# Optimization experiments

Hardware: AMD Instinct MI355X
Metric: run time of the kernel (lower is better)

## Reference

```python
import jax, jax.numpy as jnp
import numpy as np

S = 7                # feature map size
A = 12               # anchors per cell
N = S * S * A        # 588 total anchors
ANCHOR_SCALES = [0.3, 0.5, 0.7, 0.9]
ANCHOR_RATIOS = [0.7, 1.0, 1.3]
CONF_THR = 0.3
NMS_THR = 0.5
MAX_DET = 100
BN_EPS = 1e-5
DN = ('NCHW', 'OIHW', 'NCHW')


def _anchors():
    g = (jnp.arange(S, dtype=jnp.float32) + 0.5) / S
    cx, cy = jnp.meshgrid(g, g, indexing='ij')
    centers = jnp.stack([cx, cy], -1).reshape(-1, 2)                 # [49,2]
    sc = jnp.asarray(ANCHOR_SCALES, jnp.float32)[:, None]
    rt = jnp.sqrt(jnp.asarray(ANCHOR_RATIOS, jnp.float32))[None, :]
    ws = (sc * rt).reshape(-1)
    hs = (sc / rt).reshape(-1)
    deltas = jnp.stack([-ws, -hs, ws, hs], -1) * 0.5                 # [12,4]
    return (jnp.concatenate([centers, centers], -1)[:, None, :] + deltas[None]).reshape(-1, 4)


def _conv(x, w, b, pad):
    y = jax.lax.conv_general_dilated(x, w, (1, 1), [(pad, pad), (pad, pad)], dimension_numbers=DN)
    return y + b[None, :, None, None]


def _bn_relu(x, g, be, mu, var):
    inv = g * jax.lax.rsqrt(var + BN_EPS)
    return jax.nn.relu(x * inv[None, :, None, None] + (be - mu * inv)[None, :, None, None])


def _decode(box_pred, anchors):
    ac = (anchors[:, :2] + anchors[:, 2:]) * 0.5
    asz = anchors[:, 2:] - anchors[:, :2]
    pc = box_pred[..., :2] * asz + ac
    ps = jnp.exp(box_pred[..., 2:]) * asz
    return jnp.concatenate([pc - ps * 0.5, pc + ps * 0.5], -1)


def _iou(b):
    area = (b[:, 2] - b[:, 0]) * (b[:, 3] - b[:, 1])
    lt = jnp.maximum(b[:, None, :2], b[None, :, :2])
    rb = jnp.minimum(b[:, None, 2:], b[None, :, 2:])
    wh = jnp.clip(rb - lt, 0.0)
    inter = wh[..., 0] * wh[..., 1]
    return inter / (area[:, None] + area[None, :] - inter + 1e-9)


def _nms_single(boxes, scores):
    # greedy NMS, fixed-shape: sort by score, sequentially suppress, pad to MAX_DET
    order = jnp.argsort(-scores)
    bs = boxes[order]
    ss = scores[order]
    vs = ss > CONF_THR
    iou = _iou(bs)
    idx = jnp.arange(N)

    def body(suppr, i):
        keep = vs[i] & jnp.logical_not(suppr[i])
        suppr = suppr | (keep & (iou[i] > NMS_THR) & (idx > i))
        return suppr, keep

    _, keep = jax.lax.scan(body, jnp.zeros((N,), bool), idx)
    kept = jnp.where(keep, ss, -1.0)           # scores in (0,1), -1 is a safe sentinel
    top_s, top_i = jax.lax.top_k(kept, MAX_DET)
    valid = top_s > 0.0
    out_b = jnp.where(valid[:, None], bs[top_i], 0.0)
    out_s = jnp.where(valid, top_s, 0.0)
    return jnp.concatenate([out_b, out_s[:, None], valid.astype(jnp.float32)[:, None]], -1)


def _forward(features, w1, b1, g1, be1, mu1, var1, w2, b2, g2, be2, mu2, var2,
             w3, b3, g3, be3, mu3, var3, w4, b4, g4, be4, mu4, var4,
             w_cls, b_cls, w_box, b_box):
    x = _bn_relu(_conv(features, w1, b1, 0), g1, be1, mu1, var1)   # fpn 1x1
    x = _bn_relu(_conv(x, w2, b2, 1), g2, be2, mu2, var2)          # fpn 3x3
    x = _bn_relu(_conv(x, w3, b3, 1), g3, be3, mu3, var3)          # det_conv 1
    x = _bn_relu(_conv(x, w4, b4, 1), g4, be4, mu4, var4)          # det_conv 2
    B = features.shape[0]
    box = _conv(x, w_box, b_box, 1).transpose(0, 2, 3, 1).reshape(B, -1, 4)
    conf = jax.nn.sigmoid(_conv(x, w_cls, b_cls, 1)).transpose(0, 2, 3, 1).reshape(B, -1)
    boxes = _decode(box, _anchors())
    return jax.vmap(_nms_single)(boxes, conf)   # [B, MAX_DET, 6] = box(4)+score+valid


def setup_inputs() -> dict:
    key = jax.random.key(0)
    ks = iter(jax.random.split(key, 64))
    B = 256
    d = {'features': jax.random.normal(next(ks), (B, 512, S, S), jnp.float32)}
    for n, o, i, k in [('1', 256, 512, 1), ('2', 256, 256, 3), ('3', 256, 256, 3), ('4', 256, 256, 3)]:
        d['w' + n] = 0.01 * jax.random.normal(next(ks), (o, i, k, k), jnp.float32)
        d['b' + n] = jnp.zeros((o,), jnp.float32)
        d['g' + n] = 1.0 + 0.1 * jax.random.normal(next(ks), (o,), jnp.float32)
        d['be' + n] = 0.05 * jax.random.normal(next(ks), (o,), jnp.float32)
        d['mu' + n] = 0.1 * jax.random.normal(next(ks), (o,), jnp.float32)
        d['var' + n] = jax.random.uniform(next(ks), (o,), jnp.float32, 0.5, 1.5)
    d['w_cls'] = 0.01 * jax.random.normal(next(ks), (A, 256, 3, 3), jnp.float32)
    d['b_cls'] = jnp.zeros((A,), jnp.float32)
    d['w_box'] = 0.01 * jax.random.normal(next(ks), (4 * A, 256, 3, 3), jnp.float32)
    d['b_box'] = jnp.zeros((4 * A,), jnp.float32)
    return d


def reference(features, w1, b1, g1, be1, mu1, var1, w2, b2, g2, be2, mu2, var2,
              w3, b3, g3, be3, mu3, var3, w4, b4, g4, be4, mu4, var4,
              w_cls, b_cls, w_box, b_box):
    return _forward(features, w1, b1, g1, be1, mu1, var1, w2, b2, g2, be2, mu2, var2,
                    w3, b3, g3, be3, mu3, var3, w4, b4, g4, be4, mu4, var4,
                    w_cls, b_cls, w_box, b_box)
```

## Files before the change

### kernel.cpp

```cpp
#include <hip/hip_runtime.h>
#include <cmath>
#include <cstdint>

#define NPOS 49
#define NANCH 588

__global__ void transpose_all(
    const float* __restrict__ w1, const float* __restrict__ w2,
    const float* __restrict__ w3, const float* __restrict__ w4,
    const float* __restrict__ wb, const float* __restrict__ wc,
    float* __restrict__ w1t, float* __restrict__ w2t, float* __restrict__ w3t,
    float* __restrict__ w4t, float* __restrict__ wbt, float* __restrict__ wct) {
  int idx = blockIdx.x * blockDim.x + threadIdx.x;
  if (idx < 131072) {
    int o = idx / 512, c = idx % 512;
    w1t[((c >> 2) * 256 + o) * 4 + (c & 3)] = w1[idx];
    return;
  }
  idx -= 131072;
  if (idx < 589824) {
    int o = idx / 2304, ck = idx % 2304, c = ck / 9, k = ck - c * 9;
    w2t[(c * 256 + o) * 12 + k] = w2[idx]; return;
  }
  idx -= 589824;
  if (idx < 589824) {
    int o = idx / 2304, ck = idx % 2304, c = ck / 9, k = ck - c * 9;
    w3t[(c * 256 + o) * 12 + k] = w3[idx]; return;
  }
  idx -= 589824;
  if (idx < 589824) {
    int o = idx / 2304, ck = idx % 2304, c = ck / 9, k = ck - c * 9;
    w4t[(c * 256 + o) * 12 + k] = w4[idx]; return;
  }
  idx -= 589824;
  if (idx < 110592) { int o = idx / 2304, ck = idx % 2304; wbt[ck * 48 + o] = wb[idx]; return; }
  idx -= 110592;
  if (idx < 27648)  { int o = idx / 2304, ck = idx % 2304; wct[ck * 12 + o] = wc[idx]; return; }
}

__global__ __launch_bounds__(512, 1) void conv1x1_bn(
    const float* __restrict__ in, const float* __restrict__ wt_f,
    const float* __restrict__ bias, const float* __restrict__ gg,
    const float* __restrict__ be, const float* __restrict__ mu,
    const float* __restrict__ var, float* __restrict__ out) {
  __shared__ float smem[512 * 52];
  const int b = blockIdx.x, t = threadIdx.x;
  const int slot = t & 127, cg = t >> 7;
  const int o0 = slot, o1 = slot + 128;
  const float* inb = in + (size_t)b * (512 * NPOS);
  const float4* wq = (const float4*)wt_f;
  const int q0 = cg * 32;
  float4 wca = wq[q0 * 256 + o0];
  float4 wcb = wq[q0 * 256 + o1];
  for (int i = t; i < 512 * NPOS; i += 512) {
    int c = i / NPOS, p = i - c * NPOS;
    smem[c * 52 + p] = inb[i];
  }
  float acc0[NPOS], acc1[NPOS];
#pragma unroll
  for (int p = 0; p < NPOS; ++p) { acc0[p] = 0.f; acc1[p] = 0.f; }
  __syncthreads();
  for (int q = q0; q < q0 + 32; ++q) {
    int nq = (q + 1 < q0 + 32) ? q + 1 : q;
    float4 wna = wq[nq * 256 + o0];
    float4 wnb = wq[nq * 256 + o1];
#pragma unroll
    for (int j = 0; j < 4; ++j) {
      float wa = (j == 0) ? wca.x : (j == 1) ? wca.y : (j == 2) ? wca.z : wca.w;
      float wb2 = (j == 0) ? wcb.x : (j == 1) ? wcb.y : (j == 2) ? wcb.z : wcb.w;
      const float* row = smem + (q * 4 + j) * 52;
      const float4* tr = (const float4*)row;
#pragma unroll
      for (int jj = 0; jj < 12; ++jj) {
        float4 qv = tr[jj];
        acc0[4 * jj + 0] = fmaf(wa, qv.x, acc0[4 * jj + 0]);
        acc0[4 * jj + 1] = fmaf(wa, qv.y, acc0[4 * jj + 1]);
        acc0[4 * jj + 2] = fmaf(wa, qv.z, acc0[4 * jj + 2]);
        acc0[4 * jj + 3] = fmaf(wa, qv.w, acc0[4 * jj + 3]);
        acc1[4 * jj + 0] = fmaf(wb2, qv.x, acc1[4 * jj + 0]);
        acc1[4 * jj + 1] = fmaf(wb2, qv.y, acc1[4 * jj + 1]);
        acc1[4 * jj + 2] = fmaf(wb2, qv.z, acc1[4 * jj + 2]);
        acc1[4 * jj + 3] = fmaf(wb2, qv.w, acc1[4 * jj + 3]);
      }
      float s48 = row[48];
      acc0[48] = fmaf(wa, s48, acc0[48]);
      acc1[48] = fmaf(wb2, s48, acc1[48]);
    }
    wca = wna; wcb = wnb;
  }
  __syncthreads();
  float* P0 = smem;
  float* P1 = smem + 12544;
  if (cg == 1) {
#pragma unroll
    for (int p = 0; p < NPOS; ++p) { P0[(slot * 2 + 0) * NPOS + p] = acc0[p]; P0[(slot * 2 + 1) * NPOS + p] = acc1[p]; }
  }
  if (cg == 3) {
#pragma unroll
    for (int p = 0; p < NPOS; ++p) { P1[(slot * 2 + 0) * NPOS + p] = acc0[p]; P1[(slot * 2 + 1) * NPOS + p] = acc1[p]; }
  }
  __syncthreads();
  if (cg == 0) {
#pragma unroll
    for (int p = 0; p < NPOS; ++p) { acc0[p] += P0[(slot * 2 + 0) * NPOS + p]; acc1[p] += P0[(slot * 2 + 1) * NPOS + p]; }
  }
  if (cg == 2) {
#pragma unroll
    for (int p = 0; p < NPOS; ++p) { acc0[p] += P1[(slot * 2 + 0) * NPOS + p]; acc1[p] += P1[(slot * 2 + 1) * NPOS + p]; }
  }
  __syncthreads();
  if (cg == 2) {
#pragma unroll
    for (int p = 0; p < NPOS; ++p) { P0[(slot * 2 + 0) * NPOS + p] = acc0[p]; P0[(slot * 2 + 1) * NPOS + p] = acc1[p]; }
  }
  __syncthreads();
  if (cg == 0) {
    float sc0 = gg[o0] / sqrtf(var[o0] + 1e-5f);
    float ad0 = (bias[o0] - mu[o0]) * sc0 + be[o0];
    float sc1 = gg[o1] / sqrtf(var[o1] + 1e-5f);
    float ad1 = (bias[o1] - mu[o1]) * sc1 + be[o1];
#pragma unroll
    for (int p = 0; p < NPOS; ++p) {
      float v0 = (acc0[p] + P0[(slot * 2 + 0) * NPOS + p]) * sc0 + ad0;
      float v1 = (acc1[p] + P0[(slot * 2 + 1) * NPOS + p]) * sc1 + ad1;
      P1[o0 * NPOS + p] = v0 > 0.f ? v0 : 0.f;
      P1[o1 * NPOS + p] = v1 > 0.f ? v1 : 0.f;
    }
  }
  __syncthreads();
  float* outb = out + (size_t)b * (256 * NPOS);
  for (int i = t; i < 256 * NPOS; i += 512) outb[i] = P1[i];
}

#define LOADROW2(dst, base, yy)                                         \
  do {                                                                  \
    const float4* q4_ = (const float4*)((base) + (yy) * 8);             \
    float4 a_ = q4_[0], b_ = q4_[1];                                    \
    dst[0] = 0.f;                                                       \
    dst[1] = a_.x; dst[2] = a_.y; dst[3] = a_.z; dst[4] = a_.w;         \
    dst[5] = b_.x; dst[6] = b_.y; dst[7] = b_.z; dst[8] = b_.w;         \
  } while (0)

#define FMA9(accbase, rt, rc, rb)                                       \
  do {                                                                  \
    _Pragma("unroll")                                                   \
    for (int x = 0; x < 7; ++x) {                                       \
      float s = acc[(accbase) + x];                                     \
      s = fmaf(wa0.x, rt[x],     s);                                    \
      s = fmaf(wa0.y, rt[x + 1], s);                                    \
      s = fmaf(wa0.z, rt[x + 2], s);                                    \
      s = fmaf(wa0.w, rc[x],     s);                                    \
      s = fmaf(wa1.x, rc[x + 1], s);                                    \
      s = fmaf(wa1.y, rc[x + 2], s);                                    \
      s = fmaf(wa1.z, rb[x],     s);                                    \
      s = fmaf(wa1.w, rb[x + 1], s);                                    \
      s = fmaf(wa2.x, rb[x + 2], s);                                    \
      acc[(accbase) + x] = s;                                           \
    }                                                                   \
  } while (0)

__global__ __launch_bounds__(512, 2) void conv3x3_bn(
    const float* __restrict__ in, const float* __restrict__ wt,
    const float* __restrict__ bias, const float* __restrict__ gg,
    const float* __restrict__ be, const float* __restrict__ mu,
    const float* __restrict__ var, float* __restrict__ out) {
  __shared__ float smem[256 * 56];
  const int blk = blockIdx.x, t = threadIdx.x;
  const int b = blk >> 1, oh = blk & 1;
  const int slot = t & 127, cg = t >> 7;
  const int og = oh * 128 + slot;
  const float* inb = in + (size_t)b * (256 * NPOS);
  float4* z4 = (float4*)smem;
  for (int i = t; i < 3584; i += 512) z4[i] = make_float4(0.f, 0.f, 0.f, 0.f);
  const int c0 = cg * 64;
  const float4* wv4 = (const float4*)wt;
  float4 wa0 = wv4[(c0 * 256 + og) * 3 + 0];
  float4 wa1 = wv4[(c0 * 256 + og) * 3 + 1];
  float4 wa2 = wv4[(c0 * 256 + og) * 3 + 2];
  __syncthreads();
  for (int i = t; i < 256 * NPOS; i += 512) {
    int c = i / NPOS, p = i - c * NPOS, y = p / 7, x = p - y * 7;
    smem[c * 56 + y * 8 + x] = inb[i];
  }
  float acc[NPOS];
#pragma unroll
  for (int p = 0; p < NPOS; ++p) acc[p] = 0.f;
  __syncthreads();
  for (int cl = 0; cl < 64; ++cl) {
    const int c = c0 + cl;
    const int cn = (cl + 1 < 64) ? c + 1 : c;
    float4 na0 = wv4[(cn * 256 + og) * 3 + 0];
    float4 na1 = wv4[(cn * 256 + og) * 3 + 1];
    float4 na2 = wv4[(cn * 256 + og) * 3 + 2];
    const float* tb = smem + c * 56;
    float R0[9], R1[9], R2[9];
    LOADROW2(R0, tb, 0);
    LOADROW2(R1, tb, 1);
#pragma unroll
    for (int x = 0; x < 7; ++x) {
      float s = acc[x];
      s = fmaf(wa0.w, R0[x],     s);
      s = fmaf(wa1.x, R0[x + 1], s);
      s = fmaf(wa1.y, R0[x + 2], s);
      s = fmaf(wa1.z, R1[x],     s);
      s = fmaf(wa1.w, R1[x + 1], s);
      s = fmaf(wa2.x, R1[x + 2], s);
      acc[x] = s;
    }
    LOADROW2(R2, tb, 2);
    FMA9(7, R0, R1, R2);
    LOADROW2(R0, tb, 3);
    FMA9(14, R1, R2, R0);
    LOADROW2(R1, tb, 4);
    FMA9(21, R2, R0, R1);
    LOADROW2(R2, tb, 5);
    FMA9(28, R0, R1, R2);
    LOADROW2(R0, tb, 6);
    FMA9(35, R1, R2, R0);
#pragma unroll
    for (int x = 0; x < 7; ++x) {
      float s = acc[42 + x];
      s = fmaf(wa0.x, R2[x],     s);
      s = fmaf(wa0.y, R2[x + 1], s);
      s = fmaf(wa0.z, R2[x + 2], s);
      s = fmaf(wa0.w, R0[x],     s);
      s = fmaf(wa1.x, R0[x + 1], s);
      s = fmaf(wa1.y, R0[x + 2], s);
      acc[42 + x] = s;
    }
    wa0 = na0; wa1 = na1; wa2 = na2;
  }
  __syncthreads();
  float* P0 = smem;
  float* P1 = smem + 6272;
  if (cg == 1) { for (int p = 0; p < NPOS; ++p) P0[slot * NPOS + p] = acc[p]; }
  if (cg == 3) { for (int p = 0; p < NPOS; ++p) P1[slot * NPOS + p] = acc[p]; }
  __syncthreads();
  if (cg == 0) { for (int p = 0; p < NPOS; ++p) acc[p] += P0[slot * NPOS + p]; }
  if (cg == 2) { for (int p = 0; p < NPOS; ++p) acc[p] += P1[slot * NPOS + p]; }
  __syncthreads();
  if (cg == 2) { for (int p = 0; p < NPOS; ++p) P0[slot * NPOS + p] = acc[p]; }
  __syncthreads();
  if (cg == 0) {
    float scale = gg[og] / sqrtf(var[og] + 1e-5f);
    float add = (bias[og] - mu[og]) * scale + be[og];
#pragma unroll
    for (int p = 0; p < NPOS; ++p) {
      float v = (acc[p] + P0[slot * NPOS + p]) * scale + add;
      P1[slot * NPOS + p] = v > 0.f ? v : 0.f;
    }
  }
  __syncthreads();
  float* outb = out + (size_t)b * (256 * NPOS) + oh * (128 * NPOS);
  for (int i = t; i < 128 * NPOS; i += 512) outb[i] = P1[i];
}

#define LOADROW(dst, base, rr)                                          \
  do {                                                                  \
    const float4* q4_ = (const float4*)((base) + (rr) * 12);            \
    float4 q0_ = q4_[0], q1_ = q4_[1], q2_ = q4_[2];                    \
    dst[0] = q0_.x; dst[1] = q0_.y; dst[2] = q0_.z; dst[3] = q0_.w;     \
    dst[4] = q1_.x; dst[5] = q1_.y; dst[6] = q1_.z; dst[7] = q1_.w;     \
    dst[8] = q2_.x;                                                     \
  } while (0)

__global__ __launch_bounds__(512, 2) void heads_decode(
    const float* __restrict__ in, const float* __restrict__ wbt,
    const float* __restrict__ wct, const float* __restrict__ bb,
    const float* __restrict__ bc, float* __restrict__ BXg,
    float* __restrict__ SCg) {
  __shared__ float smem[256 * 108];
  const int b = blockIdx.x, t = threadIdx.x;
  for (int i = t; i < 256 * 108; i += 512) smem[i] = 0.f;
  __syncthreads();
  const float* inb = in + (size_t)b * (256 * NPOS);
  for (int i = t; i < 256 * NPOS; i += 512) {
    int c = i / NPOS, p = i - c * NPOS, y = p / 7, x = p - y * 7;
    smem[c * 108 + (y + 1) * 12 + (x + 1)] = inb[i];
  }
  __syncthreads();
  float acc[NPOS];
#pragma unroll
  for (int p = 0; p < NPOS; ++p) acc[p] = 0.f;
  int o = 0, cg = 0;
  if (t < 480) {
    o = t % 60; cg = t / 60;
    const float* wbase; int wstr;
    if (o < 48) { wbase = wbt + o; wstr = 48; }
    else        { wbase = wct + (o - 48); wstr = 12; }
    const int c0 = cg * 32;
    float wc_[9];
#pragma unroll
    for (int k = 0; k < 9; ++k) wc_[k] = wbase[(c0 * 9 + k) * wstr];
    for (int c = c0; c < c0 + 32; ++c) {
      int cn = (c + 1 < c0 + 32) ? c + 1 : c;
      float wn_[9];
#pragma unroll
      for (int k = 0; k < 9; ++k) wn_[k] = wbase[(cn * 9 + k) * wstr];
      const float* tb = smem + c * 108;
      float R[3][9];
      LOADROW(R[0], tb, 0);
      LOADROW(R[1], tb, 1);
#pragma unroll
      for (int y = 0; y < 7; ++y) {
        LOADROW(R[(y + 2) % 3], tb, y + 2);
        const float* r0 = R[y % 3];
        const float* r1 = R[(y + 1) % 3];
        const float* r2 = R[(y + 2) % 3];
#pragma unroll
        for (int x = 0; x < 7; ++x) {
          float s = acc[y * 7 + x];
          s = fmaf(wc_[0], r0[x], s);
          s = fmaf(wc_[1], r0[x + 1], s);
          s = fmaf(wc_[2], r0[x + 2], s);
          s = fmaf(wc_[3], r1[x], s);
          s = fmaf(wc_[4], r1[x + 1], s);
          s = fmaf(wc_[5], r1[x + 2], s);
          s = fmaf(wc_[6], r2[x], s);
          s = fmaf(wc_[7], r2[x + 1], s);
          s = fmaf(wc_[8], r2[x + 2], s);
          acc[y * 7 + x] = s;
        }
      }
#pragma unroll
      for (int k = 0; k < 9; ++k) wc_[k] = wn_[k];
    }
  }
  __syncthreads();
  float* part = smem;
  float* H = smem + 7 * 2940;
  if (t < 480 && cg > 0) {
#pragma unroll
    for (int p = 0; p < NPOS; ++p) part[(cg - 1) * 2940 + o * NPOS + p] = acc[p];
  }
  __syncthreads();
  if (t < 60) {
    float bsum = (o < 48) ? bb[o] : bc[o - 48];
#pragma unroll
    for (int p = 0; p < NPOS; ++p) {
      float v = acc[p] + bsum;
      for (int g = 0; g < 7; ++g) v += part[g * 2940 + o * NPOS + p];
      H[o * NPOS + p] = v;
    }
  }
  __syncthreads();
  const float scl[4] = {0.3f, 0.5f, 0.7f, 0.9f};
  const float rat[3] = {0.7f, 1.0f, 1.3f};
  for (int n = t; n < NANCH; n += 512) {
    int p = n / 12, a = n - p * 12;
    int ph = p / 7, pw = p - ph * 7;
    float cx = (ph + 0.5f) / 7.0f;
    float cy = (pw + 0.5f) / 7.0f;
    int s = a / 3, r = a - s * 3;
    float rt = sqrtf(rat[r]);
    float wsz = scl[s] * rt, hsz = scl[s] / rt;
    float x1 = cx + (-wsz) * 0.5f, y1 = cy + (-hsz) * 0.5f;
    float x2 = cx + wsz * 0.5f,    y2 = cy + hsz * 0.5f;
    float acx = (x1 + x2) * 0.5f,  acy = (y1 + y2) * 0.5f;
    float asx = x2 - x1,           asy = y2 - y1;
    float bp0 = H[(a * 4 + 0) * NPOS + p];
    float bp1 = H[(a * 4 + 1) * NPOS + p];
    float bp2 = H[(a * 4 + 2) * NPOS + p];
    float bp3 = H[(a * 4 + 3) * NPOS + p];
    float pcx = bp0 * asx + acx;
    float pcy = bp1 * asy + acy;
    float psx = expf(bp2) * asx;
    float psy = expf(bp3) * asy;
    float* bx = BXg + (size_t)b * (NANCH * 4) + n * 4;
    bx[0] = pcx - psx * 0.5f;
    bx[1] = pcy - psy * 0.5f;
    bx[2] = pcx + psx * 0.5f;
    bx[3] = pcy + psy * 0.5f;
    float lg = H[(48 + a) * NPOS + p];
    SCg[(size_t)b * NANCH + n] = 1.0f / (1.0f + expf(-lg));
  }
}

__device__ inline unsigned long long shfl64(unsigned long long v, int lane) {
  int lo = __shfl((int)(unsigned)(v & 0xffffffffULL), lane, 64);
  int hi = __shfl((int)(unsigned)(v >> 32), lane, 64);
  return ((unsigned long long)(unsigned)hi << 32) | (unsigned)lo;
}

__global__ __launch_bounds__(512, 4) void nms_kernel(
    const float* __restrict__ BXg, const float* __restrict__ SCg,
    float* __restrict__ out) {
  __shared__ float smem[16576];
  unsigned long long* KEY = (unsigned long long*)smem;
  float* SB  = smem + 1176;
  float* SSc = smem + 3528;
  float* AR  = smem + 4116;
  unsigned long long* ADJ = (unsigned long long*)(smem + 4704);
  int* KEEP = (int*)(smem + 16464);
  int* CNT  = (int*)(smem + 16564);
  const int b = blockIdx.x, t = threadIdx.x;
  const float* scb = SCg + (size_t)b * NANCH;
  const float4* bxb = (const float4*)(BXg + (size_t)b * (NANCH * 4));
  for (int i = t; i < NANCH; i += 512) {
    unsigned u = __float_as_uint(scb[i]);
    u = (u & 0x80000000u) ? ~u : (u | 0x80000000u);
    u = ~u;
    KEY[i] = ((unsigned long long)u << 32) | (unsigned)i;
  }
  __syncthreads();
  for (int i = t; i < NANCH; i += 512) {
    unsigned long long k = KEY[i];
    int rank = 0;
    for (int j = 0; j < NANCH; ++j) rank += (KEY[j] < k) ? 1 : 0;
    float4 bx = bxb[i];
    ((float4*)SB)[rank] = bx;
    SSc[rank] = scb[i];
    AR[rank] = (bx.z - bx.x) * (bx.w - bx.y);
  }
  __syncthreads();
  const float4* SB4 = (const float4*)SB;
  for (int task = t; task < NANCH * 10; task += 512) {
    int i = task % NANCH, w = task / NANCH;
    float4 a = SB4[i];
    float aar = AR[i];
    int jbase = w * 64;
    int jend = NANCH - jbase; if (jend > 64) jend = 64;
    unsigned long long bits = 0;
    for (int bi = 0; bi < jend; ++bi) {
      int j = jbase + bi;
      float4 bb = SB4[j];
      float ltx = fmaxf(a.x, bb.x), lty = fmaxf(a.y, bb.y);
      float rbx = fminf(a.z, bb.z), rby = fminf(a.w, bb.w);
      float wx = rbx - ltx; wx = wx > 0.f ? wx : 0.f;
      float wy = rby - lty; wy = wy > 0.f ? wy : 0.f;
      float inter = wx * wy;
      float iou = inter / (aar + AR[j] - inter + 1e-9f);
      if (iou > 0.5f) bits |= (1ULL << bi);
    }
    ADJ[i * 10 + w] = bits;
  }
  __syncthreads();
  if (t < 64) {
    unsigned long long valid = 0, supp = 0;
    if (t < 10) {
      int jbase = t * 64;
      int jend = NANCH - jbase; if (jend > 64) jend = 64;
      for (int k = 0; k < jend; ++k)
        valid |= (unsigned long long)(SSc[jbase + k] > 0.3f ? 1 : 0) << k;
    }
    int cnt = 0;
    for (int w = 0; w < 10 && cnt < 100; ++w) {
      unsigned long long cur = shfl64(valid, w) & ~shfl64(supp, w);
      while (cur && cnt < 100) {
        int bpos = (int)__builtin_ctzll(cur);
        int i = w * 64 + bpos;
        if (t == 0) KEEP[cnt] = i;
        cnt++;
        unsigned long long a = (t < 10) ? ADJ[i * 10 + t] : 0ULL;
        if (t < w) a = 0ULL;
        else if (t == w) a &= ~((2ULL << bpos) - 1ULL);
        supp |= a;
        unsigned long long aw = shfl64(a, w);
        cur &= ~aw;
        cur &= ~(1ULL << bpos);
      }
    }
    if (t == 0) *CNT = cnt;
  }
  __syncthreads();
  int cnt = *CNT;
  if (t < 100) {
    float4 bx = make_float4(0.f, 0.f, 0.f, 0.f);
    float s = 0.f, vld = 0.f;
    if (t < cnt) {
      int i = KEEP[t];
      bx = SB4[i];
      s = SSc[i];
      vld = 1.f;
    }
    float* ob = out + (size_t)b * 600 + t * 6;
    ob[0] = bx.x; ob[1] = bx.y; ob[2] = bx.z; ob[3] = bx.w;
    ob[4] = s;    ob[5] = vld;
  }
}

extern "C" void kernel_launch(void* const* d_in, const int* in_sizes, int n_in,
                              void* d_out, int out_size, void* d_ws, size_t ws_size,
                              hipStream_t stream) {
  const float* feat = (const float*)d_in[0];
  const float* w1  = (const float*)d_in[1];
  const float* b1  = (const float*)d_in[2];
  const float* g1  = (const float*)d_in[3];
  const float* be1 = (const float*)d_in[4];
  const float* mu1 = (const float*)d_in[5];
  const float* v1  = (const float*)d_in[6];
  const float* w2  = (const float*)d_in[7];
  const float* b2  = (const float*)d_in[8];
  const float* g2  = (const float*)d_in[9];
  const float* be2 = (const float*)d_in[10];
  const float* mu2 = (const float*)d_in[11];
  const float* v2  = (const float*)d_in[12];
  const float* w3  = (const float*)d_in[13];
  const float* b3  = (const float*)d_in[14];
  const float* g3  = (const float*)d_in[15];
  const float* be3 = (const float*)d_in[16];
  const float* mu3 = (const float*)d_in[17];
  const float* v3  = (const float*)d_in[18];
  const float* w4  = (const float*)d_in[19];
  const float* b4  = (const float*)d_in[20];
  const float* g4  = (const float*)d_in[21];
  const float* be4 = (const float*)d_in[22];
  const float* mu4 = (const float*)d_in[23];
  const float* v4  = (const float*)d_in[24];
  const float* wcls = (const float*)d_in[25];
  const float* bcls = (const float*)d_in[26];
  const float* wbox = (const float*)d_in[27];
  const float* bbox = (const float*)d_in[28];

  const int B = in_sizes[0] / (512 * NPOS);
  float* ws  = (float*)d_ws;
  size_t xsz = (size_t)B * 256 * NPOS;
  float* xa  = ws;
  float* xb  = xa + xsz;
  float* w1t = xb + xsz;
  float* w2t = w1t + 131072;
  float* w3t = w2t + 786432;
  float* w4t = w3t + 786432;
  float* wbt = w4t + 786432;
  float* wct = wbt + 110592;
  float* BXg = wct + 27648;
  float* SCg = BXg + (size_t)B * (NANCH * 4);

  transpose_all<<<(2038784 + 255) / 256, 256, 0, stream>>>(
      w1, w2, w3, w4, wbox, wcls, w1t, w2t, w3t, w4t, wbt, wct);
  conv1x1_bn<<<B, 512, 0, stream>>>(feat, w1t, b1, g1, be1, mu1, v1, xa);
  conv3x3_bn<<<2 * B, 512, 0, stream>>>(xa, w2t, b2, g2, be2, mu2, v2, xb);
  conv3x3_bn<<<2 * B, 512, 0, stream>>>(xb, w3t, b3, g3, be3, mu3, v3, xa);
  conv3x3_bn<<<2 * B, 512, 0, stream>>>(xa, w4t, b4, g4, be4, mu4, v4, xb);
  heads_decode<<<B, 512, 0, stream>>>(xb, wbt, wct, bbox, bcls, BXg, SCg);
  nms_kernel<<<B, 512, 0, stream>>>(BXg, SCg, (float*)d_out);
}
```

Measured before the change: 848.6 us.

## Split conv1x1 and heads kernels across two blocks per image, pin occupancy

The 1x1 conv is now split by output-channel half and the heads/decode kernel by spatial row half, so both launch two blocks per image instead of one. This roughly halves registers and shared memory per block. All conv kernels also get a fixed waves-per-EU occupancy attribute. The extra parallelism should fill more CUs when the batch is small. The cost is that the 1x1 conv and the heads kernel each read their input twice, and the heads reduction now needs more synchronised steps.

Result: no change. 851.5 us (+0.3%).

```diff
diff --git a/kernel.cpp b/kernel.cpp
--- a/kernel.cpp
+++ b/kernel.cpp
@@ -38,98 +38,76 @@
   if (idx < 27648)  { int o = idx / 2304, ck = idx % 2304; wct[ck * 12 + o] = wc[idx]; return; }
 }
 
-__global__ __launch_bounds__(512, 1) void conv1x1_bn(
+__global__ __launch_bounds__(512) __attribute__((amdgpu_waves_per_eu(4, 4)))
+void conv1x1_bn(
     const float* __restrict__ in, const float* __restrict__ wt_f,
     const float* __restrict__ bias, const float* __restrict__ gg,
     const float* __restrict__ be, const float* __restrict__ mu,
     const float* __restrict__ var, float* __restrict__ out) {
-  __shared__ float smem[512 * 52];
-  const int b = blockIdx.x, t = threadIdx.x;
+  __shared__ float smem[256 * 52];
+  const int blk = blockIdx.x, t = threadIdx.x;
+  const int b = blk >> 1, oh = blk & 1;
   const int slot = t & 127, cg = t >> 7;
-  const int o0 = slot, o1 = slot + 128;
+  const int og = oh * 128 + slot;
   const float* inb = in + (size_t)b * (512 * NPOS);
   const float4* wq = (const float4*)wt_f;
-  const int q0 = cg * 32;
-  float4 wca = wq[q0 * 256 + o0];
-  float4 wcb = wq[q0 * 256 + o1];
-  for (int i = t; i < 512 * NPOS; i += 512) {
-    int c = i / NPOS, p = i - c * NPOS;
-    smem[c * 52 + p] = inb[i];
-  }
-  float acc0[NPOS], acc1[NPOS];
-#pragma unroll
-  for (int p = 0; p < NPOS; ++p) { acc0[p] = 0.f; acc1[p] = 0.f; }
-  __syncthreads();
-  for (int q = q0; q < q0 + 32; ++q) {
-    int nq = (q + 1 < q0 + 32) ? q + 1 : q;
-    float4 wna = wq[nq * 256 + o0];
-    float4 wnb = wq[nq * 256 + o1];
-#pragma unroll
-    for (int j = 0; j < 4; ++j) {
-      float wa = (j == 0) ? wca.x : (j == 1) ? wca.y : (j == 2) ? wca.z : wca.w;
-      float wb2 = (j == 0) ? wcb.x : (j == 1) ? wcb.y : (j == 2) ? wcb.z : wcb.w;
-      const float* row = smem + (q * 4 + j) * 52;
-      const float4* tr = (const float4*)row;
-#pragma unroll
-      for (int jj = 0; jj < 12; ++jj) {
-        float4 qv = tr[jj];
-        acc0[4 * jj + 0] = fmaf(wa, qv.x, acc0[4 * jj + 0]);
-        acc0[4 * jj + 1] = fmaf(wa, qv.y, acc0[4 * jj + 1]);
-        acc0[4 * jj + 2] = fmaf(wa, qv.z, acc0[4 * jj + 2]);
-        acc0[4 * jj + 3] = fmaf(wa, qv.w, acc0[4 * jj + 3]);
-        acc1[4 * jj + 0] = fmaf(wb2, qv.x, acc1[4 * jj + 0]);
-        acc1[4 * jj + 1] = fmaf(wb2, qv.y, acc1[4 * jj + 1]);
-        acc1[4 * jj + 2] = fmaf(wb2, qv.z, acc1[4 * jj + 2]);
-        acc1[4 * jj + 3] = fmaf(wb2, qv.w, acc1[4 * jj + 3]);
+  float acc[NPOS];
+#pragma unroll
+  for (int p = 0; p < NPOS; ++p) acc[p] = 0.f;
+  for (int h = 0; h < 2; ++h) {
+    __syncthreads();
+    for (int i = t; i < 256 * NPOS; i += 512) {
+      int c = i / NPOS, p = i - c * NPOS;
+      smem[c * 52 + p] = inb[(h * 256 + c) * NPOS + p];
+    }
+    __syncthreads();
+    const int q0 = h * 64 + cg * 16;
+    float4 wcur = wq[q0 * 256 + og];
+    for (int q = q0; q < q0 + 16; ++q) {
+      int nq = (q + 1 < q0 + 16) ? q + 1 : q;
+      float4 wnxt = wq[nq * 256 + og];
+      const int clb = (q - h * 64) * 4;
+#pragma unroll
+      for (int j = 0; j < 4; ++j) {
+        float wv = (j == 0) ? wcur.x : (j == 1) ? wcur.y : (j == 2) ? wcur.z : wcur.w;
+        const float* row = smem + (clb + j) * 52;
+        const float4* tr = (const float4*)row;
+#pragma unroll
+        for (int jj = 0; jj < 12; ++jj) {
+          float4 qv = tr[jj];
+          acc[4 * jj + 0] = fmaf(wv, qv.x, acc[4 * jj + 0]);
+          acc[4 * jj + 1] = fmaf(wv, qv.y, acc[4 * jj + 1]);
+          acc[4 * jj + 2] = fmaf(wv, qv.z, acc[4 * jj + 2]);
+          acc[4 * jj + 3] = fmaf(wv, qv.w, acc[4 * jj + 3]);
+        }
+        acc[48] = fmaf(wv, row[48], acc[48]);
       }
-      float s48 = row[48];
-      acc0[48] = fmaf(wa, s48, acc0[48]);
-      acc1[48] = fmaf(wb2, s48, acc1[48]);
-    }
-    wca = wna; wcb = wnb;
+      wcur = wnxt;
+    }
   }
   __syncthreads();
   float* P0 = smem;
-  float* P1 = smem + 12544;
-  if (cg == 1) {
-#pragma unroll
-    for (int p = 0; p < NPOS; ++p) { P0[(slot * 2 + 0) * NPOS + p] = acc0[p]; P0[(slot * 2 + 1) * NPOS + p] = acc1[p]; }
-  }
-  if (cg == 3) {
-#pragma unroll
-    for (int p = 0; p < NPOS; ++p) { P1[(slot * 2 + 0) * NPOS + p] = acc0[p]; P1[(slot * 2 + 1) * NPOS + p] = acc1[p]; }
-  }
+  float* P1 = smem + 6272;
+  if (cg == 1) { for (int p = 0; p < NPOS; ++p) P0[slot * NPOS + p] = acc[p]; }
+  if (cg == 3) { for (int p = 0; p < NPOS; ++p) P1[slot * NPOS + p] = acc[p]; }
+  __syncthreads();
+  if (cg == 0) { for (int p = 0; p < NPOS; ++p) acc[p] += P0[slot * NPOS + p]; }
+  if (cg == 2) { for (int p = 0; p < NPOS; ++p) acc[p] += P1[slot * NPOS + p]; }
+  __syncthreads();
+  if (cg == 2) { for (int p = 0; p < NPOS; ++p) P0[slot * NPOS + p] = acc[p]; }
   __syncthreads();
   if (cg == 0) {
-#pragma unroll
-    for (int p = 0; p < NPOS; ++p) { acc0[p] += P0[(slot * 2 + 0) * NPOS + p]; acc1[p] += P0[(slot * 2 + 1) * NPOS + p]; }
-  }
-  if (cg == 2) {
-#pragma unroll
-    for (int p = 0; p < NPOS; ++p) { acc0[p] += P1[(slot * 2 + 0) * NPOS + p]; acc1[p] += P1[(slot * 2 + 1) * NPOS + p]; }
-  }
-  __syncthreads();
-  if (cg == 2) {
-#pragma unroll
-    for (int p = 0; p < NPOS; ++p) { P0[(slot * 2 + 0) * NPOS + p] = acc0[p]; P0[(slot * 2 + 1) * NPOS + p] = acc1[p]; }
-  }
-  __syncthreads();
-  if (cg == 0) {
-    float sc0 = gg[o0] / sqrtf(var[o0] + 1e-5f);
-    float ad0 = (bias[o0] - mu[o0]) * sc0 + be[o0];
-    float sc1 = gg[o1] / sqrtf(var[o1] + 1e-5f);
-    float ad1 = (bias[o1] - mu[o1]) * sc1 + be[o1];
+    float scale = gg[og] / sqrtf(var[og] + 1e-5f);
+    float add = (bias[og] - mu[og]) * scale + be[og];
 #pragma unroll
     for (int p = 0; p < NPOS; ++p) {
-      float v0 = (acc0[p] + P0[(slot * 2 + 0) * NPOS + p]) * sc0 + ad0;
-      float v1 = (acc1[p] + P0[(slot * 2 + 1) * NPOS + p]) * sc1 + ad1;
-      P1[o0 * NPOS + p] = v0 > 0.f ? v0 : 0.f;
-      P1[o1 * NPOS + p] = v1 > 0.f ? v1 : 0.f;
-    }
-  }
-  __syncthreads();
-  float* outb = out + (size_t)b * (256 * NPOS);
-  for (int i = t; i < 256 * NPOS; i += 512) outb[i] = P1[i];
+      float v = (acc[p] + P0[slot * NPOS + p]) * scale + add;
+      P1[slot * NPOS + p] = v > 0.f ? v : 0.f;
+    }
+  }
+  __syncthreads();
+  float* outb = out + (size_t)b * (256 * NPOS) + oh * (128 * NPOS);
+  for (int i = t; i < 128 * NPOS; i += 512) outb[i] = P1[i];
 }
 
 #define LOADROW2(dst, base, yy)                                         \
@@ -159,7 +137,8 @@
     }                                                                   \
   } while (0)
 
-__global__ __launch_bounds__(512, 2) void conv3x3_bn(
+__global__ __launch_bounds__(512) __attribute__((amdgpu_waves_per_eu(4, 4)))
+void conv3x3_bn(
     const float* __restrict__ in, const float* __restrict__ wt,
     const float* __restrict__ bias, const float* __restrict__ gg,
     const float* __restrict__ be, const float* __restrict__ mu,
@@ -255,33 +234,45 @@
   for (int i = t; i < 128 * NPOS; i += 512) outb[i] = P1[i];
 }
 
-#define LOADROW(dst, base, rr)                                          \
+#define HFMA9(accbase, rt, rc, rb)                                      \
   do {                                                                  \
-    const float4* q4_ = (const float4*)((base) + (rr) * 12);            \
-    float4 q0_ = q4_[0], q1_ = q4_[1], q2_ = q4_[2];                    \
-    dst[0] = q0_.x; dst[1] = q0_.y; dst[2] = q0_.z; dst[3] = q0_.w;     \
-    dst[4] = q1_.x; dst[5] = q1_.y; dst[6] = q1_.z; dst[7] = q1_.w;     \
-    dst[8] = q2_.x;                                                     \
+    _Pragma("unroll")                                                   \
+    for (int x = 0; x < 7; ++x) {                                       \
+      float s = acc[(accbase) + x];                                     \
+      s = fmaf(wc_[0], rt[x],     s);                                   \
+      s = fmaf(wc_[1], rt[x + 1], s);                                   \
+      s = fmaf(wc_[2], rt[x + 2], s);                                   \
+      s = fmaf(wc_[3], rc[x],     s);                                   \
+      s = fmaf(wc_[4], rc[x + 1], s);                                   \
+      s = fmaf(wc_[5], rc[x + 2], s);                                   \
+      s = fmaf(wc_[6], rb[x],     s);                                   \
+      s = fmaf(wc_[7], rb[x + 1], s);                                   \
+      s = fmaf(wc_[8], rb[x + 2], s);                                   \
+      acc[(accbase) + x] = s;                                           \
+    }                                                                   \
   } while (0)
 
-__global__ __launch_bounds__(512, 2) void heads_decode(
+__global__ __launch_bounds__(512) __attribute__((amdgpu_waves_per_eu(4, 4)))
+void heads_decode(
     const float* __restrict__ in, const float* __restrict__ wbt,
     const float* __restrict__ wct, const float* __restrict__ bb,
     const float* __restrict__ bc, float* __restrict__ BXg,
     float* __restrict__ SCg) {
-  __shared__ float smem[256 * 108];
-  const int b = blockIdx.x, t = threadIdx.x;
-  for (int i = t; i < 256 * 108; i += 512) smem[i] = 0.f;
+  __shared__ float smem[14720];
+  const int blk = blockIdx.x, t = threadIdx.x;
+  const int b = blk >> 1, pg = blk & 1;
+  float4* z4 = (float4*)smem;
+  for (int i = t; i < 3584; i += 512) z4[i] = make_float4(0.f, 0.f, 0.f, 0.f);
   __syncthreads();
   const float* inb = in + (size_t)b * (256 * NPOS);
   for (int i = t; i < 256 * NPOS; i += 512) {
     int c = i / NPOS, p = i - c * NPOS, y = p / 7, x = p - y * 7;
-    smem[c * 108 + (y + 1) * 12 + (x + 1)] = inb[i];
-  }
-  __syncthreads();
-  float acc[NPOS];
-#pragma unroll
-  for (int p = 0; p < NPOS; ++p) acc[p] = 0.f;
+    smem[c * 56 + y * 8 + x] = inb[i];
+  }
+  __syncthreads();
+  float acc[28];
+#pragma unroll
+  for (int p = 0; p < 28; ++p) acc[p] = 0.f;
   int o = 0, cg = 0;
   if (t < 480) {
     o = t % 60; cg = t / 60;
@@ -297,29 +288,45 @@
       float wn_[9];
 #pragma unroll
       for (int k = 0; k < 9; ++k) wn_[k] = wbase[(cn * 9 + k) * wstr];
-      const float* tb = smem + c * 108;
-      float R[3][9];
-      LOADROW(R[0], tb, 0);
-      LOADROW(R[1], tb, 1);
-#pragma unroll
-      for (int y = 0; y < 7; ++y) {
-        LOADROW(R[(y + 2) % 3], tb, y + 2);
-        const float* r0 = R[y % 3];
-        const float* r1 = R[(y + 1) % 3];
-        const float* r2 = R[(y + 2) % 3];
+      const float* tb = smem + c * 56;
+      float R0[9], R1[9], R2[9];
+      if (pg == 0) {
+        LOADROW2(R0, tb, 0);
+        LOADROW2(R1, tb, 1);
 #pragma unroll
         for (int x = 0; x < 7; ++x) {
-          float s = acc[y * 7 + x];
-          s = fmaf(wc_[0], r0[x], s);
-          s = fmaf(wc_[1], r0[x + 1], s);
-          s = fmaf(wc_[2], r0[x + 2], s);
-          s = fmaf(wc_[3], r1[x], s);
-          s = fmaf(wc_[4], r1[x + 1], s);
-          s = fmaf(wc_[5], r1[x + 2], s);
-          s = fmaf(wc_[6], r2[x], s);
-          s = fmaf(wc_[7], r2[x + 1], s);
-          s = fmaf(wc_[8], r2[x + 2], s);
-          acc[y * 7 + x] = s;
+          float s = acc[x];
+          s = fmaf(wc_[3], R0[x],     s);
+          s = fmaf(wc_[4], R0[x + 1], s);
+          s = fmaf(wc_[5], R0[x + 2], s);
+          s = fmaf(wc_[6], R1[x],     s);
+          s = fmaf(wc_[7], R1[x + 1], s);
+          s = fmaf(wc_[8], R1[x + 2], s);
+          acc[x] = s;
+        }
+        LOADROW2(R2, tb, 2);
+        HFMA9(7, R0, R1, R2);
+        LOADROW2(R0, tb, 3);
+        HFMA9(14, R1, R2, R0);
+        LOADROW2(R1, tb, 4);
+        HFMA9(21, R2, R0, R1);
+      } else {
+        LOADROW2(R0, tb, 3);
+        LOADROW2(R1, tb, 4);
+        LOADROW2(R2, tb, 5);
+        HFMA9(0, R0, R1, R2);
+        LOADROW2(R0, tb, 6);
+        HFMA9(7, R1, R2, R0);
+#pragma unroll
+        for (int x = 0; x < 7; ++x) {
+          float s = acc[14 + x];
+          s = fmaf(wc_[0], R2[x],     s);
+          s = fmaf(wc_[1], R2[x + 1], s);
+          s = fmaf(wc_[2], R2[x + 2], s);
+          s = fmaf(wc_[3], R0[x],     s);
+          s = fmaf(wc_[4], R0[x + 1], s);
+          s = fmaf(wc_[5], R0[x + 2], s);
+          acc[14 + x] = s;
         }
       }
 #pragma unroll
@@ -327,27 +334,46 @@
     }
   }
   __syncthreads();
-  float* part = smem;
-  float* H = smem + 7 * 2940;
-  if (t < 480 && cg > 0) {
-#pragma unroll
-    for (int p = 0; p < NPOS; ++p) part[(cg - 1) * 2940 + o * NPOS + p] = acc[p];
+  float* P = smem;
+  float* H = smem + 6720;
+  if (t < 480 && cg >= 4) {
+#pragma unroll
+    for (int p = 0; p < 28; ++p) P[((cg - 4) * 60 + o) * 28 + p] = acc[p];
+  }
+  __syncthreads();
+  if (t < 480 && cg < 4) {
+#pragma unroll
+    for (int p = 0; p < 28; ++p) acc[p] += P[(cg * 60 + o) * 28 + p];
+  }
+  __syncthreads();
+  if (t < 480 && (cg == 2 || cg == 3)) {
+#pragma unroll
+    for (int p = 0; p < 28; ++p) P[((cg - 2) * 60 + o) * 28 + p] = acc[p];
+  }
+  __syncthreads();
+  if (t < 480 && cg < 2) {
+#pragma unroll
+    for (int p = 0; p < 28; ++p) acc[p] += P[(cg * 60 + o) * 28 + p];
+  }
+  __syncthreads();
+  if (t < 480 && cg == 1) {
+#pragma unroll
+    for (int p = 0; p < 28; ++p) P[o * 28 + p] = acc[p];
   }
   __syncthreads();
   if (t < 60) {
     float bsum = (o < 48) ? bb[o] : bc[o - 48];
 #pragma unroll
-    for (int p = 0; p < NPOS; ++p) {
-      float v = acc[p] + bsum;
-      for (int g = 0; g < 7; ++g) v += part[g * 2940 + o * NPOS + p];
-      H[o * NPOS + p] = v;
-    }
-  }
-  __syncthreads();
+    for (int p = 0; p < 28; ++p) H[o * 28 + p] = acc[p] + P[o * 28 + p] + bsum;
+  }
+  __syncthreads();
+  const int y0 = pg ? 4 : 0;
+  const int npos = pg ? 21 : 28;
   const float scl[4] = {0.3f, 0.5f, 0.7f, 0.9f};
   const float rat[3] = {0.7f, 1.0f, 1.3f};
-  for (int n = t; n < NANCH; n += 512) {
-    int p = n / 12, a = n - p * 12;
+  if (t < npos * 12) {
+    int pl = t / 12, a = t - pl * 12;
+    int p = y0 * 7 + pl;
     int ph = p / 7, pw = p - ph * 7;
     float cx = (ph + 0.5f) / 7.0f;
     float cy = (pw + 0.5f) / 7.0f;
@@ -358,20 +384,21 @@
     float x2 = cx + wsz * 0.5f,    y2 = cy + hsz * 0.5f;
     float acx = (x1 + x2) * 0.5f,  acy = (y1 + y2) * 0.5f;
     float asx = x2 - x1,           asy = y2 - y1;
-    float bp0 = H[(a * 4 + 0) * NPOS + p];
-    float bp1 = H[(a * 4 + 1) * NPOS + p];
-    float bp2 = H[(a * 4 + 2) * NPOS + p];
-    float bp3 = H[(a * 4 + 3) * NPOS + p];
+    float bp0 = H[(a * 4 + 0) * 28 + pl];
+    float bp1 = H[(a * 4 + 1) * 28 + pl];
+    float bp2 = H[(a * 4 + 2) * 28 + pl];
+    float bp3 = H[(a * 4 + 3) * 28 + pl];
     float pcx = bp0 * asx + acx;
     float pcy = bp1 * asy + acy;
     float psx = expf(bp2) * asx;
     float psy = expf(bp3) * asy;
+    int n = p * 12 + a;
     float* bx = BXg + (size_t)b * (NANCH * 4) + n * 4;
     bx[0] = pcx - psx * 0.5f;
     bx[1] = pcy - psy * 0.5f;
     bx[2] = pcx + psx * 0.5f;
     bx[3] = pcy + psy * 0.5f;
-    float lg = H[(48 + a) * NPOS + p];
+    float lg = H[(48 + a) * 28 + pl];
     SCg[(size_t)b * NANCH + n] = 1.0f / (1.0f + expf(-lg));
   }
 }
@@ -528,10 +555,10 @@
 
   transpose_all<<<(2038784 + 255) / 256, 256, 0, stream>>>(
       w1, w2, w3, w4, wbox, wcls, w1t, w2t, w3t, w4t, wbt, wct);
-  conv1x1_bn<<<B, 512, 0, stream>>>(feat, w1t, b1, g1, be1, mu1, v1, xa);
+  conv1x1_bn<<<2 * B, 512, 0, stream>>>(feat, w1t, b1, g1, be1, mu1, v1, xa);
   conv3x3_bn<<<2 * B, 512, 0, stream>>>(xa, w2t, b2, g2, be2, mu2, v2, xb);
   conv3x3_bn<<<2 * B, 512, 0, stream>>>(xb, w3t, b3, g3, be3, mu3, v3, xa);
   conv3x3_bn<<<2 * B, 512, 0, stream>>>(xa, w4t, b4, g4, be4, mu4, v4, xb);
-  heads_decode<<<B, 512, 0, stream>>>(xb, wbt, wct, bbox, bcls, BXg, SCg);
+  heads_decode<<<2 * B, 512, 0, stream>>>(xb, wbt, wct, bbox, bcls, BXg, SCg);
   nms_kernel<<<B, 512, 0, stream>>>(BXg, SCg, (float*)d_out);
 }
```
